# Performance work log

Hardware: AMD Instinct MI355X
Metric: run time of the kernel (lower is better)

Reference implementation:

```python
import jax, jax.numpy as jnp
import numpy as np

B, N, D, P, HMUL, K = 2, 4096, 64, 64, 4, 16
H = D * HMUL  # attn_mlp hidden = 256
EPS = 1e-5


def setup_inputs() -> dict:
    key = jax.random.key(0)
    ks = jax.random.split(key, 18)
    def lin(k, fan_in, shape):
        return (jax.random.normal(k, shape, dtype=jnp.float32) / np.sqrt(fan_in)).astype(jnp.float32)
    return {
        "x": jax.random.normal(ks[0], (B, N, D), dtype=jnp.float32),
        "pos": jax.random.uniform(ks[1], (B, N, 3), dtype=jnp.float32),
        "w_qkv": lin(ks[2], D, (D, 3 * D)), "b_qkv": jnp.zeros((3 * D,), jnp.float32),
        "w_p1": lin(ks[3], 3, (3, P)),     "b_p1": jnp.zeros((P,), jnp.float32),
        "w_p2": lin(ks[4], P, (P, D)),     "b_p2": jnp.zeros((D,), jnp.float32),
        "w_a1": lin(ks[5], D, (D, H)),     "b_a1": jnp.zeros((H,), jnp.float32),
        "w_a2": lin(ks[6], H, (H, D)),     "b_a2": jnp.zeros((D,), jnp.float32),
        "w_fc": lin(ks[7], D, (D, D)),     "b_fc": jnp.zeros((D,), jnp.float32),
        "gamma": jnp.ones((D,), jnp.float32), "beta": jnp.zeros((D,), jnp.float32),
    }


def reference(x, pos, w_qkv, b_qkv, w_p1, b_p1, w_p2, b_p2,
              w_a1, b_a1, w_a2, b_a2, w_fc, b_fc, gamma, beta):
    residual = x
    qkv = x @ w_qkv + b_qkv                      # [B,N,3D]
    q, k, v = jnp.split(qkv, 3, axis=-1)         # each [B,N,D]

    # full O(N^2) pairwise distances for KNN (smallest-k)
    rel = pos[:, :, None, :] - pos[:, None, :, :]       # [B,N,N,3]
    dist = jnp.sqrt(jnp.sum(rel * rel, axis=-1))        # [B,N,N]
    _, idx = jax.lax.top_k(-dist, K)                    # [B,N,K] nearest indices

    # gather neighbors (gather commutes with the pointwise MLPs the torch
    # code applies before its neighbor_select, so math is identical)
    gather = jax.vmap(lambda arr, i: arr[i])            # arr:[N,*], i:[N,K] -> [N,K,*]
    k_nb = gather(k, idx)                               # [B,N,K,D]
    v_nb = gather(v, idx)                               # [B,N,K,D]
    pos_nb = gather(pos, idx)                           # [B,N,K,3]

    qk_map = q[:, :, None, :] - k_nb                    # [B,N,K,D]
    rel_nb = pos[:, :, None, :] - pos_nb                # [B,N,K,3]
    pos_emb = jax.nn.relu(rel_nb @ w_p1 + b_p1) @ w_p2 + b_p2   # [B,N,K,D]

    h = qk_map + pos_emb
    scores = jax.nn.relu(h @ w_a1 + b_a1) @ w_a2 + b_a2          # [B,N,K,D]
    attn = jax.nn.softmax(scores, axis=-2)                       # over K neighbors
    agg = jnp.sum(attn * v_nb, axis=-2)                          # [B,N,D]

    agg = agg @ w_fc + b_fc
    # BatchNorm1d over channel dim D (training-mode batch stats over B and N)
    mean = jnp.mean(agg, axis=(0, 1))
    var = jnp.mean(jnp.square(agg - mean), axis=(0, 1))
    agg = (agg - mean) * jax.lax.rsqrt(var + EPS) * gamma + beta
    return jax.nn.relu(agg) + residual
```

## Files before the change

### kernel.cpp

```cpp
#include <hip/hip_runtime.h>
#include <hip/hip_bf16.h>
#include <math.h>

#define NPTS 4096
#define KNB 16
#define CAP 384
#define QPB 8

typedef __attribute__((ext_vector_type(8))) short bf16x8;
typedef __attribute__((ext_vector_type(4))) float f32x4;
#define MFMA16(a, b, c) __builtin_amdgcn_mfma_f32_16x16x32_bf16(a, b, c, 0, 0, 0)

__device__ __forceinline__ unsigned short f2bf(float f) {
  unsigned int u = __float_as_uint(f);
  unsigned int r = (u + 0x7fffu + ((u >> 16) & 1u)) >> 16;
  return (unsigned short)r;
}

__global__ __launch_bounds__(256) void pack_kernel(
    const float* __restrict__ w_qkv, const float* __restrict__ w_a1,
    const float* __restrict__ w_a2, const float* __restrict__ w_p2,
    unsigned short* __restrict__ pkq, unsigned short* __restrict__ pk1,
    unsigned short* __restrict__ pk2, unsigned short* __restrict__ pkp,
    float* __restrict__ stats) {
  int e = blockIdx.x * 256 + threadIdx.x;
  if (e < 128) stats[e] = 0.f;
  if (e < 12288) {
    int j = e & 7, lane = (e >> 3) & 63, t = e >> 9;
    int ks = t & 1, nt = t >> 1;
    int k = ks * 32 + ((lane >> 4) << 3) + j, n = nt * 16 + (lane & 15);
    pkq[e] = f2bf(w_qkv[k * 192 + n]);
  } else if (e < 28672) {
    int e1 = e - 12288;
    int j = e1 & 7, lane = (e1 >> 3) & 63, t = e1 >> 9;
    int ks = t & 1, nt = t >> 1;
    int k = ks * 32 + ((lane >> 4) << 3) + j, n = nt * 16 + (lane & 15);
    pk1[e1] = f2bf(w_a1[k * 256 + n]);
  } else if (e < 45056) {
    int e2 = e - 28672;
    int j = e2 & 7, lane = (e2 >> 3) & 63, t = e2 >> 9;
    int ks = t & 7, nt = t >> 3;
    int k = ks * 32 + ((lane >> 4) << 3) + j, n = nt * 16 + (lane & 15);
    pk2[e2] = f2bf(w_a2[k * 64 + n]);
  } else if (e < 49152) {
    int e3 = e - 45056;
    int j = e3 & 7, lane = (e3 >> 3) & 63, t = e3 >> 9;
    int ks = t & 1, nt = t >> 1;
    int k = ks * 32 + ((lane >> 4) << 3) + j, n = nt * 16 + (lane & 15);
    pkp[e3] = f2bf(w_p2[k * 64 + n]);
  }
}

__global__ __launch_bounds__(256) void qkv_kernel(
    const float* __restrict__ x, const unsigned short* __restrict__ pkq,
    const float* __restrict__ b_qkv, float* __restrict__ qkv) {
  int tid = threadIdx.x, lane = tid & 63, w = tid >> 6;
  int m = lane & 15, quad = lane >> 4;
  int r0 = blockIdx.x * 16;

  const float* xr = x + (size_t)(r0 + m) * 64;
  float xa[8], xb[8];
  *(float4*)&xa[0] = *(const float4*)(xr + quad * 8);
  *(float4*)&xa[4] = *(const float4*)(xr + quad * 8 + 4);
  *(float4*)&xb[0] = *(const float4*)(xr + 32 + quad * 8);
  *(float4*)&xb[4] = *(const float4*)(xr + 32 + quad * 8 + 4);
  bf16x8 a0, a1;
#pragma unroll
  for (int j = 0; j < 8; ++j) {
    a0[j] = (short)f2bf(xa[j]);
    a1[j] = (short)f2bf(xb[j]);
  }

#pragma unroll
  for (int t = 0; t < 3; ++t) {
    int nt = w * 3 + t;
    bf16x8 b0 = *(const bf16x8*)(pkq + ((size_t)(nt * 2 + 0) * 64 + lane) * 8);
    bf16x8 b1 = *(const bf16x8*)(pkq + ((size_t)(nt * 2 + 1) * 64 + lane) * 8);
    int n = nt * 16 + m;
    f32x4 acc = {0.f, 0.f, 0.f, 0.f};
    acc = MFMA16(a0, b0, acc);
    acc = MFMA16(a1, b1, acc);
    float bb = b_qkv[n];
#pragma unroll
    for (int i = 0; i < 4; ++i)
      qkv[(size_t)(r0 + quad * 4 + i) * 192 + n] = acc[i] + bb;
  }
}

__global__ __launch_bounds__(256, 4) void fused_kernel(
    const float* __restrict__ qkv, const float* __restrict__ pos,
    const unsigned short* __restrict__ pk1,
    const unsigned short* __restrict__ pk2,
    const unsigned short* __restrict__ pkp, const float* __restrict__ w_p1,
    const float* __restrict__ b_p1, const float* __restrict__ b_p2,
    const float* __restrict__ b_a1, const float* __restrict__ b_a2,
    const float* __restrict__ w_fc, const float* __restrict__ b_fc,
    float* __restrict__ y, float* __restrict__ stats) {
  __shared__ __align__(16) char smem[25216];
  __shared__ int s_idx[128];

  int tid = threadIdx.x, lane = tid & 63, w = tid >> 6;
  int m = lane & 15, quad = lane >> 4;
  int g0 = blockIdx.x * QPB;
  int b = g0 >> 12;
  const float* posb = pos + (size_t)b * NPTS * 3;

  {
    unsigned int(*cbits)[CAP] = (unsigned int(*)[CAP])smem;
    int(*cidx)[CAP] = (int(*)[CAP])(smem + 12288);
    unsigned long long* wmin = (unsigned long long*)(smem + 24576);
    float* sretry = (float*)(smem + 24608);
    unsigned int* scnt = (unsigned int*)(smem + 24640);
    unsigned long long* sprev = (unsigned long long*)(smem + 24672);
    int* sany = (int*)(smem + 24680);
    float* st2 = (float*)(smem + 24688);

    float qx[QPB], qy[QPB], qz[QPB], t2q[QPB];
#pragma unroll
    for (int q = 0; q < QPB; ++q) {
      int i = (g0 + q) & (NPTS - 1);
      qx[q] = posb[i * 3 + 0];
      qy[q] = posb[i * 3 + 1];
      qz[q] = posb[i * 3 + 2];
    }
    if (tid < QPB) {
      int i = (g0 + tid) & (NPTS - 1);
      float ax = posb[i * 3 + 0], ay = posb[i * 3 + 1], az = posb[i * 3 + 2];
      float r = 0.131f;
#pragma unroll
      for (int it = 0; it < 3; ++it) {
        float inv2r = 0.5f / r;
        float fx = (fminf(ax + r, 1.f) - fmaxf(ax - r, 0.f)) * inv2r;
        float fy = (fminf(ay + r, 1.f) - fmaxf(ay - r, 0.f)) * inv2r;
        float fz = (fminf(az + r, 1.f) - fmaxf(az - r, 0.f)) * inv2r;
        float expn = 17157.28f * r * r * r * fx * fy * fz;
        float s = exp2f(0.33333334f * log2f(38.f / expn));
        s = fminf(fmaxf(s, 0.7f), 1.6f);
        r = fminf(r * s, 0.32f);
      }
      st2[tid] = r * r;
      scnt[tid] = 0;
    }
    if (tid == 0) sany[0] = 0;
    __syncthreads();
#pragma unroll
    for (int q = 0; q < QPB; ++q) t2q[q] = st2[q];

    for (int c = 0; c < NPTS / 256; ++c) {
      int j = c * 256 + tid;
      int j3 = j * 3;
      float px = posb[j3 + 0], py = posb[j3 + 1], pz = posb[j3 + 2];
#pragma unroll
      for (int q = 0; q < QPB; ++q) {
        float dx = qx[q] - px, dy = qy[q] - py, dz = qz[q] - pz;
        float d2 = fmaf(dz, dz, fmaf(dy, dy, dx * dx));
        bool hit = d2 < t2q[q];
        unsigned long long mask = __ballot(hit);
        if (mask) {
          if (hit) {
            unsigned int p = atomicAdd(&scnt[q], 1u);
            if (p < CAP) {
              cbits[q][p] = __float_as_uint(d2);
              cidx[q][p] = j;
            }
          }
        }
      }
    }
    __syncthreads();

    if (tid < QPB) {
      int q = tid;
      unsigned int n = scnt[q];
      float nt = 0.f;
      if (n < KNB) nt = st2[q] * 4.f;
      else if (n > CAP) nt = st2[q] * 0.4f;
      sretry[q] = nt;
      if (nt != 0.f) {
        scnt[q] = 0;
        sany[0] = 1;
      }
    }
    __syncthreads();

    if (sany[0]) {
      float tr[QPB];
#pragma unroll
      for (int q = 0; q < QPB; ++q) tr[q] = sretry[q];
      for (int c = 0; c < NPTS / 256; ++c) {
        int j = c * 256 + tid;
        int j3 = j * 3;
        float px = posb[j3 + 0], py = posb[j3 + 1], pz = posb[j3 + 2];
#pragma unroll
        for (int q = 0; q < QPB; ++q) {
          if (tr[q] != 0.f) {
            float dx = qx[q] - px, dy = qy[q] - py, dz = qz[q] - pz;
            float d2 = fmaf(dz, dz, fmaf(dy, dy, dx * dx));
            bool hit = d2 < tr[q];
            unsigned long long mask = __ballot(hit);
            if (mask) {
              if (hit) {
                unsigned int p = atomicAdd(&scnt[q], 1u);
                if (p < CAP) {
                  cbits[q][p] = __float_as_uint(d2);
                  cidx[q][p] = j;
                }
              }
            }
          }
        }
      }
      __syncthreads();
    }

    for (int qq = 0; qq < 2; ++qq) {
      int q = w * 2 + qq;
      int L = (int)scnt[q];
      if (L >= KNB && L <= CAP) {
        for (int i = lane; i < L; i += 64) {
          unsigned long long ki = ((unsigned long long)cbits[q][i] << 32) |
                                  (unsigned int)cidx[q][i];
          int rank = 0;
          for (int mm = 0; mm < L; ++mm) {
            unsigned long long km = ((unsigned long long)cbits[q][mm] << 32) |
                                    (unsigned int)cidx[q][mm];
            rank += km < ki;
          }
          if (rank < KNB) s_idx[q * KNB + rank] = cidx[q][i];
        }
      }
    }
    __syncthreads();

    for (int q = 0; q < QPB; ++q) {
      unsigned int n = scnt[q];
      if (n < KNB || n > CAP) {
        unsigned long long prev = 0ull;
        for (int r = 0; r < KNB; ++r) {
          unsigned long long best = ~0ull;
          for (int c = 0; c < NPTS / 256; ++c) {
            int j = c * 256 + tid;
            float dx = qx[q] - posb[j * 3 + 0];
            float dy = qy[q] - posb[j * 3 + 1];
            float dz = qz[q] - posb[j * 3 + 2];
            float d2 = fmaf(dz, dz, fmaf(dy, dy, dx * dx));
            unsigned long long key =
                ((unsigned long long)__float_as_uint(d2) << 32) |
                (unsigned int)j;
            bool ok = (r == 0) || (key > prev);
            best = (ok && key < best) ? key : best;
          }
#pragma unroll
          for (int off = 32; off > 0; off >>= 1) {
            unsigned long long o = __shfl_down(best, off);
            best = best < o ? best : o;
          }
          if (lane == 0) wmin[w] = best;
          __syncthreads();
          if (tid == 0) {
            unsigned long long m0 = wmin[0], m1 = wmin[1];
            unsigned long long m2 = wmin[2], m3 = wmin[3];
            unsigned long long a = m0 < m1 ? m0 : m1;
            unsigned long long d = m2 < m3 ? m2 : m3;
            a = a < d ? a : d;
            s_idx[q * KNB + r] = (int)(unsigned int)a;
            sprev[0] = a;
          }
          __syncthreads();
          prev = sprev[0];
          __syncthreads();
        }
      }
    }
  }
  __syncthreads();

  unsigned short(*region)[72] = (unsigned short(*)[72])smem;
  float(*s_rel)[32][3] = (float(*)[32][3])(smem + 18432);

  if (lane < 32) {
    int row = 32 * w + lane;
    int p = lane >> 4;
    int g = g0 + 2 * w + p;
    int jb = (b << 12) | s_idx[row];
    s_rel[w][lane][0] = pos[(size_t)g * 3 + 0] - pos[(size_t)jb * 3 + 0];
    s_rel[w][lane][1] = pos[(size_t)g * 3 + 1] - pos[(size_t)jb * 3 + 1];
    s_rel[w][lane][2] = pos[(size_t)g * 3 + 2] - pos[(size_t)jb * 3 + 2];
  }

  {
    float w0 = w_p1[lane], w1 = w_p1[64 + lane], w2 = w_p1[128 + lane];
    float bp = b_p1[lane];
    for (int rl = 0; rl < 32; ++rl) {
      int row = 32 * w + rl;
      float rx = s_rel[w][rl][0], ry = s_rel[w][rl][1], rz = s_rel[w][rl][2];
      float e = fmaf(rz, w2, fmaf(ry, w1, fmaf(rx, w0, bp)));
      region[row][lane] = f2bf(fmaxf(e, 0.f));
    }
  }

  {
    bf16x8 ea0[2], ea1[2];
#pragma unroll
    for (int p = 0; p < 2; ++p) {
      ea0[p] = *(const bf16x8*)&region[32 * w + 16 * p + m][quad * 8];
      ea1[p] = *(const bf16x8*)&region[32 * w + 16 * p + m][32 + quad * 8];
    }
#pragma unroll
    for (int nt = 0; nt < 4; ++nt) {
      bf16x8 b0 = *(const bf16x8*)(pkp + ((size_t)(nt * 2 + 0) * 64 + lane) * 8);
      bf16x8 b1 = *(const bf16x8*)(pkp + ((size_t)(nt * 2 + 1) * 64 + lane) * 8);
      int col = nt * 16 + m;
      float bp2 = b_p2[col];
#pragma unroll
      for (int p = 0; p < 2; ++p) {
        f32x4 acc = {0.f, 0.f, 0.f, 0.f};
        acc = MFMA16(ea0[p], b0, acc);
        acc = MFMA16(ea1[p], b1, acc);
        int g = g0 + 2 * w + p;
        float qv = qkv[(size_t)g * 192 + col];
#pragma unroll
        for (int i = 0; i < 4; ++i) {
          int row = 32 * w + 16 * p + quad * 4 + i;
          int jb = (b << 12) | s_idx[row];
          float kv = qkv[(size_t)jb * 192 + 64 + col];
          region[row][col] = f2bf(qv - kv + acc[i] + bp2);
        }
      }
    }
  }

  float vreg[2][4][4];
#pragma unroll
  for (int p = 0; p < 2; ++p)
#pragma unroll
    for (int i = 0; i < 4; ++i) {
      int row = 32 * w + 16 * p + quad * 4 + i;
      int jb = (b << 12) | s_idx[row];
      const float* vr = qkv + (size_t)jb * 192 + 128;
#pragma unroll
      for (int nt2 = 0; nt2 < 4; ++nt2) vreg[p][nt2][i] = vr[nt2 * 16 + m];
    }

  bf16x8 ha0[2], ha1[2];
#pragma unroll
  for (int p = 0; p < 2; ++p) {
    ha0[p] = *(const bf16x8*)&region[32 * w + 16 * p + m][quad * 8];
    ha1[p] = *(const bf16x8*)&region[32 * w + 16 * p + m][32 + quad * 8];
  }
  f32x4 acc2[2][4];
#pragma unroll
  for (int p = 0; p < 2; ++p)
#pragma unroll
    for (int nt2 = 0; nt2 < 4; ++nt2) acc2[p][nt2] = (f32x4){0.f, 0.f, 0.f, 0.f};

  unsigned short(*s_tc)[72] = (unsigned short(*)[72])(smem + w * 4608);

#pragma unroll
  for (int c = 0; c < 4; ++c) {
#pragma unroll
    for (int ntc = 0; ntc < 4; ++ntc) {
      int nt = 4 * c + ntc;
      bf16x8 b0 = *(const bf16x8*)(pk1 + ((size_t)(nt * 2 + 0) * 64 + lane) * 8);
      bf16x8 b1 = *(const bf16x8*)(pk1 + ((size_t)(nt * 2 + 1) * 64 + lane) * 8);
      int coll = ntc * 16 + m;
      float ba = b_a1[nt * 16 + m];
#pragma unroll
      for (int p = 0; p < 2; ++p) {
        f32x4 t = {0.f, 0.f, 0.f, 0.f};
        t = MFMA16(ha0[p], b0, t);
        t = MFMA16(ha1[p], b1, t);
#pragma unroll
        for (int i = 0; i < 4; ++i)
          s_tc[16 * p + quad * 4 + i][coll] = f2bf(fmaxf(t[i] + ba, 0.f));
      }
    }
#pragma unroll
    for (int sub = 0; sub < 2; ++sub) {
      int ks = c * 2 + sub;
      bf16x8 a[2];
#pragma unroll
      for (int p = 0; p < 2; ++p)
        a[p] = *(const bf16x8*)&s_tc[16 * p + m][sub * 32 + quad * 8];
#pragma unroll
      for (int nt2 = 0; nt2 < 4; ++nt2) {
        bf16x8 bb =
            *(const bf16x8*)(pk2 + ((size_t)(nt2 * 8 + ks) * 64 + lane) * 8);
#pragma unroll
        for (int p = 0; p < 2; ++p) acc2[p][nt2] = MFMA16(a[p], bb, acc2[p][nt2]);
      }
    }
  }

  float ba2[4];
#pragma unroll
  for (int nt2 = 0; nt2 < 4; ++nt2) ba2[nt2] = b_a2[nt2 * 16 + m];
  float aggv[2][4];
#pragma unroll
  for (int p = 0; p < 2; ++p) {
#pragma unroll
    for (int nt2 = 0; nt2 < 4; ++nt2) {
      float sc[4];
#pragma unroll
      for (int i = 0; i < 4; ++i) sc[i] = acc2[p][nt2][i] + ba2[nt2];
      float mx = fmaxf(fmaxf(sc[0], sc[1]), fmaxf(sc[2], sc[3]));
      mx = fmaxf(mx, __shfl_xor(mx, 16));
      mx = fmaxf(mx, __shfl_xor(mx, 32));
      float ex[4], ss = 0.f;
#pragma unroll
      for (int i = 0; i < 4; ++i) {
        ex[i] = exp2f((sc[i] - mx) * 1.4426950408889634f);
        ss += ex[i];
      }
      ss += __shfl_xor(ss, 16);
      ss += __shfl_xor(ss, 32);
      float nu = 0.f;
#pragma unroll
      for (int i = 0; i < 4; ++i) nu = fmaf(ex[i], vreg[p][nt2][i], nu);
      nu += __shfl_xor(nu, 16);
      nu += __shfl_xor(nu, 32);
      aggv[p][nt2] = nu / ss;
    }
  }
  __syncthreads();

  float* s_agg = (float*)smem;
  if (quad == 0) {
#pragma unroll
    for (int p = 0; p < 2; ++p)
#pragma unroll
      for (int nt2 = 0; nt2 < 4; ++nt2)
        s_agg[(2 * w + p) * 64 + nt2 * 16 + m] = aggv[p][nt2];
  }
  __syncthreads();

  {
    int c = lane, r = w;
    float acc0 = b_fc[c], acc1 = b_fc[c];
    for (int d = 0; d < 64; ++d) {
      float wv = w_fc[d * 64 + c];
      acc0 = fmaf(s_agg[r * 64 + d], wv, acc0);
      acc1 = fmaf(s_agg[(r + 4) * 64 + d], wv, acc1);
    }
    y[(size_t)(g0 + r) * 64 + c] = acc0;
    y[(size_t)(g0 + r + 4) * 64 + c] = acc1;
    float* s_red = (float*)(smem + 2048);
    float* s_red2 = (float*)(smem + 3072);
    s_red[w * 64 + c] = acc0 + acc1;
    s_red2[w * 64 + c] = acc0 * acc0 + acc1 * acc1;
  }
  __syncthreads();
  if (tid < 64) {
    float* s_red = (float*)(smem + 2048);
    float* s_red2 = (float*)(smem + 3072);
    float s = s_red[tid] + s_red[64 + tid] + s_red[128 + tid] + s_red[192 + tid];
    float s2 =
        s_red2[tid] + s_red2[64 + tid] + s_red2[128 + tid] + s_red2[192 + tid];
    atomicAdd(&stats[tid], s);
    atomicAdd(&stats[64 + tid], s2);
  }
}

__global__ __launch_bounds__(256) void bn_kernel(
    const float* __restrict__ y, const float* __restrict__ x,
    const float* __restrict__ stats, const float* __restrict__ gamma,
    const float* __restrict__ beta, float* __restrict__ out) {
  size_t o = (size_t)blockIdx.x * 256 + threadIdx.x;
  int c = (int)(o & 63);
  const float inv_n = 1.f / 8192.f;
  float mean = stats[c] * inv_n;
  float var = stats[64 + c] * inv_n - mean * mean;
  float inv = rsqrtf(var + 1e-5f);
  float v = (y[o] - mean) * inv * gamma[c] + beta[c];
  out[o] = fmaxf(v, 0.f) + x[o];
}

extern "C" void kernel_launch(void* const* d_in, const int* in_sizes, int n_in,
                              void* d_out, int out_size, void* d_ws,
                              size_t ws_size, hipStream_t stream) {
  const float* x = (const float*)d_in[0];
  const float* pos = (const float*)d_in[1];
  const float* w_qkv = (const float*)d_in[2];
  const float* b_qkv = (const float*)d_in[3];
  const float* w_p1 = (const float*)d_in[4];
  const float* b_p1 = (const float*)d_in[5];
  const float* w_p2 = (const float*)d_in[6];
  const float* b_p2 = (const float*)d_in[7];
  const float* w_a1 = (const float*)d_in[8];
  const float* b_a1 = (const float*)d_in[9];
  const float* w_a2 = (const float*)d_in[10];
  const float* b_a2 = (const float*)d_in[11];
  const float* w_fc = (const float*)d_in[12];
  const float* b_fc = (const float*)d_in[13];
  const float* gamma = (const float*)d_in[14];
  const float* beta = (const float*)d_in[15];

  char* ws = (char*)d_ws;
  float* qkv = (float*)(ws + 0);
  float* y = (float*)(ws + 8912896);
  float* stats = (float*)(ws + 11010048);
  unsigned short* pk1 = (unsigned short*)(ws + 11010560);
  unsigned short* pk2 = (unsigned short*)(ws + 11043328);
  unsigned short* pkp = (unsigned short*)(ws + 11076096);
  unsigned short* pkq = (unsigned short*)(ws + 11084288);

  hipLaunchKernelGGL(pack_kernel, dim3(192), dim3(256), 0, stream, w_qkv,
                     w_a1, w_a2, w_p2, pkq, pk1, pk2, pkp, stats);
  hipLaunchKernelGGL(qkv_kernel, dim3(512), dim3(256), 0, stream, x, pkq,
                     b_qkv, qkv);
  hipLaunchKernelGGL(fused_kernel, dim3(1024), dim3(256), 0, stream, qkv, pos,
                     pk1, pk2, pkp, w_p1, b_p1, b_p2, b_a1, b_a2, w_fc, b_fc,
                     y, stats);
  hipLaunchKernelGGL(bn_kernel, dim3(2048), dim3(256), 0, stream, y, x, stats,
                     gamma, beta, (float*)d_out);
}
```

Baseline: 150.1 us.

## Split fused KNN+attention kernel into separate KNN and attention kernels

Splits the single fused kernel into a KNN kernel that writes neighbor indices to global workspace and an attention kernel that reads them. The attention kernel now handles 4 queries per block instead of 8, with smaller shared memory and register arrays, and launches twice as many blocks. The aim is to stop the large KNN shared-memory footprint from limiting attention-phase occupancy and to raise parallelism. The cost is an extra launch, a global round trip for the indices, and less reuse of the weight tile loads per block.

```diff
diff --git a/kernel.cpp b/kernel.cpp
--- a/kernel.cpp
+++ b/kernel.cpp
@@ -6,6 +6,7 @@
 #define KNB 16
 #define CAP 384
 #define QPB 8
+#define QPA 4
 
 typedef __attribute__((ext_vector_type(8))) short bf16x8;
 typedef __attribute__((ext_vector_type(4))) float f32x4;
@@ -87,201 +88,213 @@
   }
 }
 
-__global__ __launch_bounds__(256, 4) void fused_kernel(
+__global__ __launch_bounds__(256, 4) void knn_kernel(
+    const float* __restrict__ pos, int* __restrict__ knn_idx) {
+  __shared__ __align__(16) char smem[24720];
+  __shared__ int s_idx[128];
+
+  int tid = threadIdx.x, lane = tid & 63, w = tid >> 6;
+  int g0 = blockIdx.x * QPB;
+  int b = g0 >> 12;
+  const float* posb = pos + (size_t)b * NPTS * 3;
+
+  unsigned int(*cbits)[CAP] = (unsigned int(*)[CAP])smem;
+  int(*cidx)[CAP] = (int(*)[CAP])(smem + 12288);
+  unsigned long long* wmin = (unsigned long long*)(smem + 24576);
+  float* sretry = (float*)(smem + 24608);
+  unsigned int* scnt = (unsigned int*)(smem + 24640);
+  unsigned long long* sprev = (unsigned long long*)(smem + 24672);
+  int* sany = (int*)(smem + 24680);
+  float* st2 = (float*)(smem + 24688);
+
+  float qx[QPB], qy[QPB], qz[QPB], t2q[QPB];
+#pragma unroll
+  for (int q = 0; q < QPB; ++q) {
+    int i = (g0 + q) & (NPTS - 1);
+    qx[q] = posb[i * 3 + 0];
+    qy[q] = posb[i * 3 + 1];
+    qz[q] = posb[i * 3 + 2];
+  }
+  if (tid < QPB) {
+    int i = (g0 + tid) & (NPTS - 1);
+    float ax = posb[i * 3 + 0], ay = posb[i * 3 + 1], az = posb[i * 3 + 2];
+    float r = 0.131f;
+#pragma unroll
+    for (int it = 0; it < 3; ++it) {
+      float inv2r = 0.5f / r;
+      float fx = (fminf(ax + r, 1.f) - fmaxf(ax - r, 0.f)) * inv2r;
+      float fy = (fminf(ay + r, 1.f) - fmaxf(ay - r, 0.f)) * inv2r;
+      float fz = (fminf(az + r, 1.f) - fmaxf(az - r, 0.f)) * inv2r;
+      float expn = 17157.28f * r * r * r * fx * fy * fz;
+      float s = exp2f(0.33333334f * log2f(38.f / expn));
+      s = fminf(fmaxf(s, 0.7f), 1.6f);
+      r = fminf(r * s, 0.32f);
+    }
+    st2[tid] = r * r;
+    scnt[tid] = 0;
+  }
+  if (tid == 0) sany[0] = 0;
+  __syncthreads();
+#pragma unroll
+  for (int q = 0; q < QPB; ++q) t2q[q] = st2[q];
+
+  for (int c = 0; c < NPTS / 256; ++c) {
+    int j = c * 256 + tid;
+    int j3 = j * 3;
+    float px = posb[j3 + 0], py = posb[j3 + 1], pz = posb[j3 + 2];
+#pragma unroll
+    for (int q = 0; q < QPB; ++q) {
+      float dx = qx[q] - px, dy = qy[q] - py, dz = qz[q] - pz;
+      float d2 = fmaf(dz, dz, fmaf(dy, dy, dx * dx));
+      bool hit = d2 < t2q[q];
+      unsigned long long mask = __ballot(hit);
+      if (mask) {
+        if (hit) {
+          unsigned int p = atomicAdd(&scnt[q], 1u);
+          if (p < CAP) {
+            cbits[q][p] = __float_as_uint(d2);
+            cidx[q][p] = j;
+          }
+        }
+      }
+    }
+  }
+  __syncthreads();
+
+  if (tid < QPB) {
+    int q = tid;
+    unsigned int n = scnt[q];
+    float nt = 0.f;
+    if (n < KNB) nt = st2[q] * 4.f;
+    else if (n > CAP) nt = st2[q] * 0.4f;
+    sretry[q] = nt;
+    if (nt != 0.f) {
+      scnt[q] = 0;
+      sany[0] = 1;
+    }
+  }
+  __syncthreads();
+
+  if (sany[0]) {
+    float tr[QPB];
+#pragma unroll
+    for (int q = 0; q < QPB; ++q) tr[q] = sretry[q];
+    for (int c = 0; c < NPTS / 256; ++c) {
+      int j = c * 256 + tid;
+      int j3 = j * 3;
+      float px = posb[j3 + 0], py = posb[j3 + 1], pz = posb[j3 + 2];
+#pragma unroll
+      for (int q = 0; q < QPB; ++q) {
+        if (tr[q] != 0.f) {
+          float dx = qx[q] - px, dy = qy[q] - py, dz = qz[q] - pz;
+          float d2 = fmaf(dz, dz, fmaf(dy, dy, dx * dx));
+          bool hit = d2 < tr[q];
+          unsigned long long mask = __ballot(hit);
+          if (mask) {
+            if (hit) {
+              unsigned int p = atomicAdd(&scnt[q], 1u);
+              if (p < CAP) {
+                cbits[q][p] = __float_as_uint(d2);
+                cidx[q][p] = j;
+              }
+            }
+          }
+        }
+      }
+    }
+    __syncthreads();
+  }
+
+  for (int qq = 0; qq < 2; ++qq) {
+    int q = w * 2 + qq;
+    int L = (int)scnt[q];
+    if (L >= KNB && L <= CAP) {
+      for (int i = lane; i < L; i += 64) {
+        unsigned long long ki = ((unsigned long long)cbits[q][i] << 32) |
+                                (unsigned int)cidx[q][i];
+        int rank = 0;
+        for (int mm = 0; mm < L; ++mm) {
+          unsigned long long km = ((unsigned long long)cbits[q][mm] << 32) |
+                                  (unsigned int)cidx[q][mm];
+          rank += km < ki;
+        }
+        if (rank < KNB) s_idx[q * KNB + rank] = cidx[q][i];
+      }
+    }
+  }
+  __syncthreads();
+
+  for (int q = 0; q < QPB; ++q) {
+    unsigned int n = scnt[q];
+    if (n < KNB || n > CAP) {
+      unsigned long long prev = 0ull;
+      for (int r = 0; r < KNB; ++r) {
+        unsigned long long best = ~0ull;
+        for (int c = 0; c < NPTS / 256; ++c) {
+          int j = c * 256 + tid;
+          float dx = qx[q] - posb[j * 3 + 0];
+          float dy = qy[q] - posb[j * 3 + 1];
+          float dz = qz[q] - posb[j * 3 + 2];
+          float d2 = fmaf(dz, dz, fmaf(dy, dy, dx * dx));
+          unsigned long long key =
+              ((unsigned long long)__float_as_uint(d2) << 32) |
+              (unsigned int)j;
+          bool ok = (r == 0) || (key > prev);
+          best = (ok && key < best) ? key : best;
+        }
+#pragma unroll
+        for (int off = 32; off > 0; off >>= 1) {
+          unsigned long long o = __shfl_down(best, off);
+          best = best < o ? best : o;
+        }
+        if (lane == 0) wmin[w] = best;
+        __syncthreads();
+        if (tid == 0) {
+          unsigned long long m0 = wmin[0], m1 = wmin[1];
+          unsigned long long m2 = wmin[2], m3 = wmin[3];
+          unsigned long long a = m0 < m1 ? m0 : m1;
+          unsigned long long d = m2 < m3 ? m2 : m3;
+          a = a < d ? a : d;
+          s_idx[q * KNB + r] = (int)(unsigned int)a;
+          sprev[0] = a;
+        }
+        __syncthreads();
+        prev = sprev[0];
+        __syncthreads();
+      }
+    }
+  }
+  __syncthreads();
+
+  if (tid < 128) knn_idx[blockIdx.x * 128 + tid] = s_idx[tid];
+}
+
+__global__ __launch_bounds__(256, 4) void attn_kernel(
     const float* __restrict__ qkv, const float* __restrict__ pos,
-    const unsigned short* __restrict__ pk1,
+    const int* __restrict__ knn_idx, const unsigned short* __restrict__ pk1,
     const unsigned short* __restrict__ pk2,
     const unsigned short* __restrict__ pkp, const float* __restrict__ w_p1,
     const float* __restrict__ b_p1, const float* __restrict__ b_p2,
     const float* __restrict__ b_a1, const float* __restrict__ b_a2,
     const float* __restrict__ w_fc, const float* __restrict__ b_fc,
     float* __restrict__ y, float* __restrict__ stats) {
-  __shared__ __align__(16) char smem[25216];
-  __shared__ int s_idx[128];
+  __shared__ __align__(16) char smem[9984];
+  __shared__ int s_idx[64];
 
   int tid = threadIdx.x, lane = tid & 63, w = tid >> 6;
   int m = lane & 15, quad = lane >> 4;
-  int g0 = blockIdx.x * QPB;
+  int g0 = blockIdx.x * QPA;
   int b = g0 >> 12;
-  const float* posb = pos + (size_t)b * NPTS * 3;
-
-  {
-    unsigned int(*cbits)[CAP] = (unsigned int(*)[CAP])smem;
-    int(*cidx)[CAP] = (int(*)[CAP])(smem + 12288);
-    unsigned long long* wmin = (unsigned long long*)(smem + 24576);
-    float* sretry = (float*)(smem + 24608);
-    unsigned int* scnt = (unsigned int*)(smem + 24640);
-    unsigned long long* sprev = (unsigned long long*)(smem + 24672);
-    int* sany = (int*)(smem + 24680);
-    float* st2 = (float*)(smem + 24688);
-
-    float qx[QPB], qy[QPB], qz[QPB], t2q[QPB];
-#pragma unroll
-    for (int q = 0; q < QPB; ++q) {
-      int i = (g0 + q) & (NPTS - 1);
-      qx[q] = posb[i * 3 + 0];
-      qy[q] = posb[i * 3 + 1];
-      qz[q] = posb[i * 3 + 2];
-    }
-    if (tid < QPB) {
-      int i = (g0 + tid) & (NPTS - 1);
-      float ax = posb[i * 3 + 0], ay = posb[i * 3 + 1], az = posb[i * 3 + 2];
-      float r = 0.131f;
-#pragma unroll
-      for (int it = 0; it < 3; ++it) {
-        float inv2r = 0.5f / r;
-        float fx = (fminf(ax + r, 1.f) - fmaxf(ax - r, 0.f)) * inv2r;
-        float fy = (fminf(ay + r, 1.f) - fmaxf(ay - r, 0.f)) * inv2r;
-        float fz = (fminf(az + r, 1.f) - fmaxf(az - r, 0.f)) * inv2r;
-        float expn = 17157.28f * r * r * r * fx * fy * fz;
-        float s = exp2f(0.33333334f * log2f(38.f / expn));
-        s = fminf(fmaxf(s, 0.7f), 1.6f);
-        r = fminf(r * s, 0.32f);
-      }
-      st2[tid] = r * r;
-      scnt[tid] = 0;
-    }
-    if (tid == 0) sany[0] = 0;
-    __syncthreads();
-#pragma unroll
-    for (int q = 0; q < QPB; ++q) t2q[q] = st2[q];
-
-    for (int c = 0; c < NPTS / 256; ++c) {
-      int j = c * 256 + tid;
-      int j3 = j * 3;
-      float px = posb[j3 + 0], py = posb[j3 + 1], pz = posb[j3 + 2];
-#pragma unroll
-      for (int q = 0; q < QPB; ++q) {
-        float dx = qx[q] - px, dy = qy[q] - py, dz = qz[q] - pz;
-        float d2 = fmaf(dz, dz, fmaf(dy, dy, dx * dx));
-        bool hit = d2 < t2q[q];
-        unsigned long long mask = __ballot(hit);
-        if (mask) {
-          if (hit) {
-            unsigned int p = atomicAdd(&scnt[q], 1u);
-            if (p < CAP) {
-              cbits[q][p] = __float_as_uint(d2);
-              cidx[q][p] = j;
-            }
-          }
-        }
-      }
-    }
-    __syncthreads();
-
-    if (tid < QPB) {
-      int q = tid;
-      unsigned int n = scnt[q];
-      float nt = 0.f;
-      if (n < KNB) nt = st2[q] * 4.f;
-      else if (n > CAP) nt = st2[q] * 0.4f;
-      sretry[q] = nt;
-      if (nt != 0.f) {
-        scnt[q] = 0;
-        sany[0] = 1;
-      }
-    }
-    __syncthreads();
-
-    if (sany[0]) {
-      float tr[QPB];
-#pragma unroll
-      for (int q = 0; q < QPB; ++q) tr[q] = sretry[q];
-      for (int c = 0; c < NPTS / 256; ++c) {
-        int j = c * 256 + tid;
-        int j3 = j * 3;
-        float px = posb[j3 + 0], py = posb[j3 + 1], pz = posb[j3 + 2];
-#pragma unroll
-        for (int q = 0; q < QPB; ++q) {
-          if (tr[q] != 0.f) {
-            float dx = qx[q] - px, dy = qy[q] - py, dz = qz[q] - pz;
-            float d2 = fmaf(dz, dz, fmaf(dy, dy, dx * dx));
-            bool hit = d2 < tr[q];
-            unsigned long long mask = __ballot(hit);
-            if (mask) {
-              if (hit) {
-                unsigned int p = atomicAdd(&scnt[q], 1u);
-                if (p < CAP) {
-                  cbits[q][p] = __float_as_uint(d2);
-                  cidx[q][p] = j;
-                }
-              }
-            }
-          }
-        }
-      }
-      __syncthreads();
-    }
-
-    for (int qq = 0; qq < 2; ++qq) {
-      int q = w * 2 + qq;
-      int L = (int)scnt[q];
-      if (L >= KNB && L <= CAP) {
-        for (int i = lane; i < L; i += 64) {
-          unsigned long long ki = ((unsigned long long)cbits[q][i] << 32) |
-                                  (unsigned int)cidx[q][i];
-          int rank = 0;
-          for (int mm = 0; mm < L; ++mm) {
-            unsigned long long km = ((unsigned long long)cbits[q][mm] << 32) |
-                                    (unsigned int)cidx[q][mm];
-            rank += km < ki;
-          }
-          if (rank < KNB) s_idx[q * KNB + rank] = cidx[q][i];
-        }
-      }
-    }
-    __syncthreads();
-
-    for (int q = 0; q < QPB; ++q) {
-      unsigned int n = scnt[q];
-      if (n < KNB || n > CAP) {
-        unsigned long long prev = 0ull;
-        for (int r = 0; r < KNB; ++r) {
-          unsigned long long best = ~0ull;
-          for (int c = 0; c < NPTS / 256; ++c) {
-            int j = c * 256 + tid;
-            float dx = qx[q] - posb[j * 3 + 0];
-            float dy = qy[q] - posb[j * 3 + 1];
-            float dz = qz[q] - posb[j * 3 + 2];
-            float d2 = fmaf(dz, dz, fmaf(dy, dy, dx * dx));
-            unsigned long long key =
-                ((unsigned long long)__float_as_uint(d2) << 32) |
-                (unsigned int)j;
-            bool ok = (r == 0) || (key > prev);
-            best = (ok && key < best) ? key : best;
-          }
-#pragma unroll
-          for (int off = 32; off > 0; off >>= 1) {
-            unsigned long long o = __shfl_down(best, off);
-            best = best < o ? best : o;
-          }
-          if (lane == 0) wmin[w] = best;
-          __syncthreads();
-          if (tid == 0) {
-            unsigned long long m0 = wmin[0], m1 = wmin[1];
-            unsigned long long m2 = wmin[2], m3 = wmin[3];
-            unsigned long long a = m0 < m1 ? m0 : m1;
-            unsigned long long d = m2 < m3 ? m2 : m3;
-            a = a < d ? a : d;
-            s_idx[q * KNB + r] = (int)(unsigned int)a;
-            sprev[0] = a;
-          }
-          __syncthreads();
-          prev = sprev[0];
-          __syncthreads();
-        }
-      }
-    }
-  }
+
+  if (tid < 64) s_idx[tid] = knn_idx[blockIdx.x * 64 + tid];
   __syncthreads();
 
   unsigned short(*region)[72] = (unsigned short(*)[72])smem;
-  float(*s_rel)[32][3] = (float(*)[32][3])(smem + 18432);
-
-  if (lane < 32) {
-    int row = 32 * w + lane;
-    int p = lane >> 4;
-    int g = g0 + 2 * w + p;
+  float(*s_rel)[16][3] = (float(*)[16][3])(smem + 9216);
+
+  if (lane < 16) {
+    int row = 16 * w + lane;
+    int g = g0 + w;
     int jb = (b << 12) | s_idx[row];
     s_rel[w][lane][0] = pos[(size_t)g * 3 + 0] - pos[(size_t)jb * 3 + 0];
     s_rel[w][lane][1] = pos[(size_t)g * 3 + 1] - pos[(size_t)jb * 3 + 1];
@@ -291,8 +304,8 @@
   {
     float w0 = w_p1[lane], w1 = w_p1[64 + lane], w2 = w_p1[128 + lane];
     float bp = b_p1[lane];
-    for (int rl = 0; rl < 32; ++rl) {
-      int row = 32 * w + rl;
+    for (int rl = 0; rl < 16; ++rl) {
+      int row = 16 * w + rl;
       float rx = s_rel[w][rl][0], ry = s_rel[w][rl][1], rz = s_rel[w][rl][2];
       float e = fmaf(rz, w2, fmaf(ry, w1, fmaf(rx, w0, bp)));
       region[row][lane] = f2bf(fmaxf(e, 0.f));
@@ -300,61 +313,46 @@
   }
 
   {
-    bf16x8 ea0[2], ea1[2];
-#pragma unroll
-    for (int p = 0; p < 2; ++p) {
-      ea0[p] = *(const bf16x8*)&region[32 * w + 16 * p + m][quad * 8];
-      ea1[p] = *(const bf16x8*)&region[32 * w + 16 * p + m][32 + quad * 8];
-    }
+    bf16x8 ea0 = *(const bf16x8*)&region[16 * w + m][quad * 8];
+    bf16x8 ea1 = *(const bf16x8*)&region[16 * w + m][32 + quad * 8];
+    int g = g0 + w;
 #pragma unroll
     for (int nt = 0; nt < 4; ++nt) {
       bf16x8 b0 = *(const bf16x8*)(pkp + ((size_t)(nt * 2 + 0) * 64 + lane) * 8);
       bf16x8 b1 = *(const bf16x8*)(pkp + ((size_t)(nt * 2 + 1) * 64 + lane) * 8);
       int col = nt * 16 + m;
       float bp2 = b_p2[col];
-#pragma unroll
-      for (int p = 0; p < 2; ++p) {
-        f32x4 acc = {0.f, 0.f, 0.f, 0.f};
-        acc = MFMA16(ea0[p], b0, acc);
-        acc = MFMA16(ea1[p], b1, acc);
-        int g = g0 + 2 * w + p;
-        float qv = qkv[(size_t)g * 192 + col];
-#pragma unroll
-        for (int i = 0; i < 4; ++i) {
-          int row = 32 * w + 16 * p + quad * 4 + i;
-          int jb = (b << 12) | s_idx[row];
-          float kv = qkv[(size_t)jb * 192 + 64 + col];
-          region[row][col] = f2bf(qv - kv + acc[i] + bp2);
-        }
+      f32x4 acc = {0.f, 0.f, 0.f, 0.f};
+      acc = MFMA16(ea0, b0, acc);
+      acc = MFMA16(ea1, b1, acc);
+      float qv = qkv[(size_t)g * 192 + col];
+#pragma unroll
+      for (int i = 0; i < 4; ++i) {
+        int row = 16 * w + quad * 4 + i;
+        int jb = (b << 12) | s_idx[row];
+        float kv = qkv[(size_t)jb * 192 + 64 + col];
+        region[row][col] = f2bf(qv - kv + acc[i] + bp2);
       }
     }
   }
 
-  float vreg[2][4][4];
-#pragma unroll
-  for (int p = 0; p < 2; ++p)
-#pragma unroll
-    for (int i = 0; i < 4; ++i) {
-      int row = 32 * w + 16 * p + quad * 4 + i;
-      int jb = (b << 12) | s_idx[row];
-      const float* vr = qkv + (size_t)jb * 192 + 128;
-#pragma unroll
-      for (int nt2 = 0; nt2 < 4; ++nt2) vreg[p][nt2][i] = vr[nt2 * 16 + m];
-    }
-
-  bf16x8 ha0[2], ha1[2];
-#pragma unroll
-  for (int p = 0; p < 2; ++p) {
-    ha0[p] = *(const bf16x8*)&region[32 * w + 16 * p + m][quad * 8];
-    ha1[p] = *(const bf16x8*)&region[32 * w + 16 * p + m][32 + quad * 8];
-  }
-  f32x4 acc2[2][4];
-#pragma unroll
-  for (int p = 0; p < 2; ++p)
-#pragma unroll
-    for (int nt2 = 0; nt2 < 4; ++nt2) acc2[p][nt2] = (f32x4){0.f, 0.f, 0.f, 0.f};
-
-  unsigned short(*s_tc)[72] = (unsigned short(*)[72])(smem + w * 4608);
+  float vreg[4][4];
+#pragma unroll
+  for (int i = 0; i < 4; ++i) {
+    int row = 16 * w + quad * 4 + i;
+    int jb = (b << 12) | s_idx[row];
+    const float* vr = qkv + (size_t)jb * 192 + 128;
+#pragma unroll
+    for (int nt2 = 0; nt2 < 4; ++nt2) vreg[nt2][i] = vr[nt2 * 16 + m];
+  }
+
+  bf16x8 ha0 = *(const bf16x8*)&region[16 * w + m][quad * 8];
+  bf16x8 ha1 = *(const bf16x8*)&region[16 * w + m][32 + quad * 8];
+  f32x4 acc2[4];
+#pragma unroll
+  for (int nt2 = 0; nt2 < 4; ++nt2) acc2[nt2] = (f32x4){0.f, 0.f, 0.f, 0.f};
+
+  unsigned short(*s_tc)[72] = (unsigned short(*)[72])(smem + w * 2304);
 
 #pragma unroll
   for (int c = 0; c < 4; ++c) {
@@ -365,29 +363,22 @@
       bf16x8 b1 = *(const bf16x8*)(pk1 + ((size_t)(nt * 2 + 1) * 64 + lane) * 8);
       int coll = ntc * 16 + m;
       float ba = b_a1[nt * 16 + m];
-#pragma unroll
-      for (int p = 0; p < 2; ++p) {
-        f32x4 t = {0.f, 0.f, 0.f, 0.f};
-        t = MFMA16(ha0[p], b0, t);
-        t = MFMA16(ha1[p], b1, t);
-#pragma unroll
-        for (int i = 0; i < 4; ++i)
-          s_tc[16 * p + quad * 4 + i][coll] = f2bf(fmaxf(t[i] + ba, 0.f));
-      }
+      f32x4 t = {0.f, 0.f, 0.f, 0.f};
+      t = MFMA16(ha0, b0, t);
+      t = MFMA16(ha1, b1, t);
+#pragma unroll
+      for (int i = 0; i < 4; ++i)
+        s_tc[quad * 4 + i][coll] = f2bf(fmaxf(t[i] + ba, 0.f));
     }
 #pragma unroll
     for (int sub = 0; sub < 2; ++sub) {
       int ks = c * 2 + sub;
-      bf16x8 a[2];
-#pragma unroll
-      for (int p = 0; p < 2; ++p)
-        a[p] = *(const bf16x8*)&s_tc[16 * p + m][sub * 32 + quad * 8];
+      bf16x8 a = *(const bf16x8*)&s_tc[m][sub * 32 + quad * 8];
 #pragma unroll
       for (int nt2 = 0; nt2 < 4; ++nt2) {
         bf16x8 bb =
             *(const bf16x8*)(pk2 + ((size_t)(nt2 * 8 + ks) * 64 + lane) * 8);
-#pragma unroll
-        for (int p = 0; p < 2; ++p) acc2[p][nt2] = MFMA16(a[p], bb, acc2[p][nt2]);
+        acc2[nt2] = MFMA16(a, bb, acc2[nt2]);
       }
     }
   }
@@ -395,64 +386,55 @@
   float ba2[4];
 #pragma unroll
   for (int nt2 = 0; nt2 < 4; ++nt2) ba2[nt2] = b_a2[nt2 * 16 + m];
-  float aggv[2][4];
-#pragma unroll
-  for (int p = 0; p < 2; ++p) {
-#pragma unroll
-    for (int nt2 = 0; nt2 < 4; ++nt2) {
-      float sc[4];
-#pragma unroll
-      for (int i = 0; i < 4; ++i) sc[i] = acc2[p][nt2][i] + ba2[nt2];
-      float mx = fmaxf(fmaxf(sc[0], sc[1]), fmaxf(sc[2], sc[3]));
-      mx = fmaxf(mx, __shfl_xor(mx, 16));
-      mx = fmaxf(mx, __shfl_xor(mx, 32));
-      float ex[4], ss = 0.f;
-#pragma unroll
-      for (int i = 0; i < 4; ++i) {
-        ex[i] = exp2f((sc[i] - mx) * 1.4426950408889634f);
-        ss += ex[i];
-      }
-      ss += __shfl_xor(ss, 16);
-      ss += __shfl_xor(ss, 32);
-      float nu = 0.f;
-#pragma unroll
-      for (int i = 0; i < 4; ++i) nu = fmaf(ex[i], vreg[p][nt2][i], nu);
-      nu += __shfl_xor(nu, 16);
-      nu += __shfl_xor(nu, 32);
-      aggv[p][nt2] = nu / ss;
-    }
+  float aggv[4];
+#pragma unroll
+  for (int nt2 = 0; nt2 < 4; ++nt2) {
+    float sc[4];
+#pragma unroll
+    for (int i = 0; i < 4; ++i) sc[i] = acc2[nt2][i] + ba2[nt2];
+    float mx = fmaxf(fmaxf(sc[0], sc[1]), fmaxf(sc[2], sc[3]));
+    mx = fmaxf(mx, __shfl_xor(mx, 16));
+    mx = fmaxf(mx, __shfl_xor(mx, 32));
+    float ex[4], ss = 0.f;
+#pragma unroll
+    for (int i = 0; i < 4; ++i) {
+      ex[i] = exp2f((sc[i] - mx) * 1.4426950408889634f);
+      ss += ex[i];
+    }
+    ss += __shfl_xor(ss, 16);
+    ss += __shfl_xor(ss, 32);
+    float nu = 0.f;
+#pragma unroll
+    for (int i = 0; i < 4; ++i) nu = fmaf(ex[i], vreg[nt2][i], nu);
+    nu += __shfl_xor(nu, 16);
+    nu += __shfl_xor(nu, 32);
+    aggv[nt2] = nu / ss;
   }
   __syncthreads();
 
   float* s_agg = (float*)smem;
   if (quad == 0) {
 #pragma unroll
-    for (int p = 0; p < 2; ++p)
-#pragma unroll
-      for (int nt2 = 0; nt2 < 4; ++nt2)
-        s_agg[(2 * w + p) * 64 + nt2 * 16 + m] = aggv[p][nt2];
+    for (int nt2 = 0; nt2 < 4; ++nt2)
+      s_agg[w * 64 + nt2 * 16 + m] = aggv[nt2];
   }
   __syncthreads();
 
   {
     int c = lane, r = w;
-    float acc0 = b_fc[c], acc1 = b_fc[c];
-    for (int d = 0; d < 64; ++d) {
-      float wv = w_fc[d * 64 + c];
-      acc0 = fmaf(s_agg[r * 64 + d], wv, acc0);
-      acc1 = fmaf(s_agg[(r + 4) * 64 + d], wv, acc1);
-    }
+    float acc0 = b_fc[c];
+    for (int d = 0; d < 64; ++d)
+      acc0 = fmaf(s_agg[r * 64 + d], w_fc[d * 64 + c], acc0);
     y[(size_t)(g0 + r) * 64 + c] = acc0;
-    y[(size_t)(g0 + r + 4) * 64 + c] = acc1;
-    float* s_red = (float*)(smem + 2048);
-    float* s_red2 = (float*)(smem + 3072);
-    s_red[w * 64 + c] = acc0 + acc1;
-    s_red2[w * 64 + c] = acc0 * acc0 + acc1 * acc1;
+    float* s_red = (float*)(smem + 1024);
+    float* s_red2 = (float*)(smem + 2048);
+    s_red[w * 64 + c] = acc0;
+    s_red2[w * 64 + c] = acc0 * acc0;
   }
   __syncthreads();
   if (tid < 64) {
-    float* s_red = (float*)(smem + 2048);
-    float* s_red2 = (float*)(smem + 3072);
+    float* s_red = (float*)(smem + 1024);
+    float* s_red2 = (float*)(smem + 2048);
     float s = s_red[tid] + s_red[64 + tid] + s_red[128 + tid] + s_red[192 + tid];
     float s2 =
         s_red2[tid] + s_red2[64 + tid] + s_red2[128 + tid] + s_red2[192 + tid];
@@ -497,6 +479,7 @@
 
   char* ws = (char*)d_ws;
   float* qkv = (float*)(ws + 0);
+  int* knn_idx = (int*)(ws + 6291456);
   float* y = (float*)(ws + 8912896);
   float* stats = (float*)(ws + 11010048);
   unsigned short* pk1 = (unsigned short*)(ws + 11010560);
@@ -508,9 +491,11 @@
                      w_a1, w_a2, w_p2, pkq, pk1, pk2, pkp, stats);
   hipLaunchKernelGGL(qkv_kernel, dim3(512), dim3(256), 0, stream, x, pkq,
                      b_qkv, qkv);
-  hipLaunchKernelGGL(fused_kernel, dim3(1024), dim3(256), 0, stream, qkv, pos,
-                     pk1, pk2, pkp, w_p1, b_p1, b_p2, b_a1, b_a2, w_fc, b_fc,
-                     y, stats);
+  hipLaunchKernelGGL(knn_kernel, dim3(1024), dim3(256), 0, stream, pos,
+                     knn_idx);
+  hipLaunchKernelGGL(attn_kernel, dim3(2048), dim3(256), 0, stream, qkv, pos,
+                     knn_idx, pk1, pk2, pkp, w_p1, b_p1, b_p2, b_a1, b_a2,
+                     w_fc, b_fc, y, stats);
   hipLaunchKernelGGL(bn_kernel, dim3(2048), dim3(256), 0, stream, y, x, stats,
                      gamma, beta, (float*)d_out);
 }
```

New measurement: 180.8 us. 1.2x slower.
